# Kernel tuning notes

Measured on AMD Instinct MI355X. Metric: run time of the kernel, lower is better.

Reference implementation:

```python
import jax, jax.numpy as jnp
import numpy as np

N_TOKENS = 524288
D = 128          # input_dim == output_dim (output = zeros_like(x))
E = 8            # num_experts


def setup_inputs() -> dict:
    key = jax.random.key(0)
    ks = jax.random.split(key, 5)
    s = 1.0 / np.sqrt(D)
    x = jax.random.normal(ks[0], (N_TOKENS, D), dtype=jnp.float32)
    gate_W = jax.random.uniform(ks[1], (E, D), jnp.float32, -s, s)   # Linear(D, E) weight [out,in]
    gate_b = jax.random.uniform(ks[2], (E,), jnp.float32, -s, s)
    W = jax.random.uniform(ks[3], (E, D, D), jnp.float32, -s, s)     # per-expert Linear weight [E, out, in]
    b = jax.random.uniform(ks[4], (E, D), jnp.float32, -s, s)
    return {"x": x, "gate_W": gate_W, "gate_b": gate_b, "W": W, "b": b}


def reference(x, gate_W, gate_b, W, b):
    # gate_scores: [N, E]
    g = jax.nn.softmax(x @ gate_W.T + gate_b, axis=-1)
    # top-2 expert mask per token: [N, E] float {0,1}
    _, top2 = jax.lax.top_k(g, 2)                                   # [N, 2] int
    mask = jnp.zeros_like(g).at[jnp.arange(x.shape[0])[:, None], top2].set(1.0)
    # Faithful to the loop: out = sum_e g[:,e] * ((mask_e * x) @ W_e^T + b_e)
    # contraction term:   einsum over expert e and feature d
    out = jnp.einsum('ne,nd,efd->nf', g * mask, x, W)
    out = out + g @ b                                               # bias term: every expert's bias, weighted by gate
    return out
```

## Files before the change

### kernel.cpp

```cpp
#include <hip/hip_runtime.h>


typedef _Float16 half8 __attribute__((ext_vector_type(8)));
typedef float    f32x4 __attribute__((ext_vector_type(4)));

#define N_TOK   524288
#define TPB     256

__global__ __launch_bounds__(512, 2)
void moe_fused(const float* __restrict__ x,
               const float* __restrict__ gW,
               const float* __restrict__ gb,
               const float* __restrict__ W,
               const float* __restrict__ b,
               float* __restrict__ out)
{
    const int tid  = threadIdx.x;
    const int lane = tid & 63;
    const int wid  = tid >> 6;
    const int wm   = wid >> 1;
    const int wn   = wid & 1;
    const int r16  = lane & 15;
    const int q    = lane >> 4;

    const int  t0w = wm * 64;
    const long tb  = (long)blockIdx.x * TPB;

    __shared__ __align__(16) float     gW_s[8 * 128];
    __shared__             float       gb_s[8];
    __shared__ __align__(16) float     c_s[8][256];
    __shared__ __align__(16) _Float16  gA_s[256 * 32];
    __shared__ __align__(16) _Float16  bB_s[128 * 32];
    __shared__ __align__(16) _Float16  wb_s[2][128 * 128];

    ((float2*)gW_s)[tid] = ((const float2*)gW)[tid];
    if (tid < 8) gb_s[tid] = gb[tid];
    for (int i = tid; i < 128 * 32; i += 512) {
        int f = i >> 5, k = i & 31;
        bB_s[i] = (k < 8) ? (_Float16)b[k * 128 + f] : (_Float16)0.f;
    }
    __syncthreads();

    f32x4 st[4][2];
    {
        const f32x4* wsrc = (const f32x4*)W;
        #pragma unroll
        for (int it = 0; it < 4; ++it) {
            int v = it * 512 + tid;
            st[it][0] = wsrc[v * 2 + 0];
            st[it][1] = wsrc[v * 2 + 1];
        }
    }

    half8 af[4][4];
    float plog[4][8];
    #pragma unroll
    for (int m = 0; m < 4; ++m)
        #pragma unroll
        for (int e = 0; e < 8; ++e) plog[m][e] = 0.f;

    #pragma unroll
    for (int m = 0; m < 4; ++m) {
        const long tok = tb + t0w + m * 16 + r16;
        const float* xr = x + tok * 128;
        #pragma unroll
        for (int k = 0; k < 4; ++k) {
            const int col = k * 32 + q * 8;
            f32x4 v0 = *(const f32x4*)(xr + col);
            f32x4 v1 = *(const f32x4*)(xr + col + 4);
            half8 pk;
            pk[0]=(_Float16)v0[0]; pk[1]=(_Float16)v0[1]; pk[2]=(_Float16)v0[2]; pk[3]=(_Float16)v0[3];
            pk[4]=(_Float16)v1[0]; pk[5]=(_Float16)v1[1]; pk[6]=(_Float16)v1[2]; pk[7]=(_Float16)v1[3];
            af[m][k] = pk;
            #pragma unroll
            for (int e = 0; e < 8; ++e) {
                const float* g = gW_s + e * 128 + col;
                plog[m][e] += v0[0]*g[0] + v0[1]*g[1] + v0[2]*g[2] + v0[3]*g[3]
                            + v1[0]*g[4] + v1[1]*g[5] + v1[2]*g[6] + v1[3]*g[7];
            }
        }
    }

    #pragma unroll
    for (int m = 0; m < 4; ++m) {
        #pragma unroll
        for (int e = 0; e < 8; ++e) {
            float v = plog[m][e];
            v += __shfl_xor(v, 16, 64);
            v += __shfl_xor(v, 32, 64);
            plog[m][e] = v + gb_s[e];
        }
        float m1 = -1e30f; int i1 = 0;
        #pragma unroll
        for (int e = 0; e < 8; ++e) if (plog[m][e] > m1) { m1 = plog[m][e]; i1 = e; }
        float m2 = -1e30f; int i2 = (i1 == 0) ? 1 : 0;
        #pragma unroll
        for (int e = 0; e < 8; ++e) if (e != i1 && plog[m][e] > m2) { m2 = plog[m][e]; i2 = e; }
        float ge[8]; float sum = 0.f;
        #pragma unroll
        for (int e = 0; e < 8; ++e) { ge[e] = __expf(plog[m][e] - m1); sum += ge[e]; }
        const float inv = 1.f / sum;
        if (q == 0 && wn == 0) {
            const int row = t0w + m * 16 + r16;
            half8 pg;
            #pragma unroll
            for (int e = 0; e < 8; ++e) {
                float gg = ge[e] * inv;
                c_s[e][row] = (e == i1 || e == i2) ? gg : 0.f;
                pg[e] = (_Float16)gg;
            }
            half8* gp = (half8*)&gA_s[row * 32];
            half8 z8 = {0,0,0,0,0,0,0,0};
            gp[0] = pg; gp[1] = z8; gp[2] = z8; gp[3] = z8;
        }
    }
    __syncthreads();

    f32x4 acc[4][4];
    const f32x4 zq = {0.f, 0.f, 0.f, 0.f};
    {
        half8 ga[4];
        #pragma unroll
        for (int m = 0; m < 4; ++m)
            ga[m] = *(const half8*)&gA_s[(t0w + m * 16 + r16) * 32 + q * 8];
        #pragma unroll
        for (int n = 0; n < 4; ++n) {
            const half8 bf = *(const half8*)&bB_s[(wn * 64 + n * 16 + r16) * 32 + q * 8];
            #pragma unroll
            for (int m = 0; m < 4; ++m)
                acc[m][n] = __builtin_amdgcn_mfma_f32_16x16x32_f16(ga[m], bf, zq, 0, 0, 0);
        }
    }

    #pragma unroll
    for (int it = 0; it < 4; ++it) {
        int v = it * 512 + tid;
        int f = v >> 4, slot = v & 15;
        char* dst = (char*)wb_s[0] + f * 256 + ((slot * 16) ^ ((f & 7) << 4));
        half8 pk;
        pk[0]=(_Float16)st[it][0][0]; pk[1]=(_Float16)st[it][0][1];
        pk[2]=(_Float16)st[it][0][2]; pk[3]=(_Float16)st[it][0][3];
        pk[4]=(_Float16)st[it][1][0]; pk[5]=(_Float16)st[it][1][1];
        pk[6]=(_Float16)st[it][1][2]; pk[7]=(_Float16)st[it][1][3];
        *(half8*)dst = pk;
    }
    __syncthreads();

    for (int e = 0; e < 8; ++e) {
        _Float16* wcur = wb_s[e & 1];
        _Float16* wnxt = wb_s[(e & 1) ^ 1];

        if (e < 7) {
            const f32x4* wsrc = (const f32x4*)(W + (long)(e + 1) * 16384);
            #pragma unroll
            for (int it = 0; it < 4; ++it) {
                int v = it * 512 + tid;
                st[it][0] = wsrc[v * 2 + 0];
                st[it][1] = wsrc[v * 2 + 1];
            }
        }

        f32x4 cv[4];
        #pragma unroll
        for (int m = 0; m < 4; ++m)
            cv[m] = *(const f32x4*)&c_s[e][t0w + m * 16 + q * 4];

        #pragma unroll
        for (int n = 0; n < 4; ++n) {
            const int fbase = wn * 64 + n * 16 + r16;
            const char* wrow = (const char*)wcur + fbase * 256;
            const int sw = (fbase & 7) << 4;
            f32x4 tmp[4];
            #pragma unroll
            for (int k = 0; k < 4; ++k) {
                const half8 bf = *(const half8*)(wrow + ((k * 64 + q * 16) ^ sw));
                #pragma unroll
                for (int m = 0; m < 4; ++m)
                    tmp[m] = __builtin_amdgcn_mfma_f32_16x16x32_f16(
                                 af[m][k], bf, (k == 0) ? zq : tmp[m], 0, 0, 0);
            }
            #pragma unroll
            for (int m = 0; m < 4; ++m) {
                acc[m][n][0] += cv[m][0] * tmp[m][0];
                acc[m][n][1] += cv[m][1] * tmp[m][1];
                acc[m][n][2] += cv[m][2] * tmp[m][2];
                acc[m][n][3] += cv[m][3] * tmp[m][3];
            }
        }

        if (e < 7) {
            #pragma unroll
            for (int it = 0; it < 4; ++it) {
                int v = it * 512 + tid;
                int f = v >> 4, slot = v & 15;
                char* dst = (char*)wnxt + f * 256 + ((slot * 16) ^ ((f & 7) << 4));
                half8 pk;
                pk[0]=(_Float16)st[it][0][0]; pk[1]=(_Float16)st[it][0][1];
                pk[2]=(_Float16)st[it][0][2]; pk[3]=(_Float16)st[it][0][3];
                pk[4]=(_Float16)st[it][1][0]; pk[5]=(_Float16)st[it][1][1];
                pk[6]=(_Float16)st[it][1][2]; pk[7]=(_Float16)st[it][1][3];
                *(half8*)dst = pk;
            }
            __syncthreads();
        }
    }

    #pragma unroll
    for (int m = 0; m < 4; ++m) {
        const long trow = tb + t0w + m * 16 + q * 4;
        #pragma unroll
        for (int r = 0; r < 4; ++r) {
            float* orow = out + (trow + r) * 128 + wn * 64 + r16;
            orow[0]  = acc[m][0][r];
            orow[16] = acc[m][1][r];
            orow[32] = acc[m][2][r];
            orow[48] = acc[m][3][r];
        }
    }
}

extern "C" void kernel_launch(void* const* d_in, const int* in_sizes, int n_in,
                              void* d_out, int out_size, void* d_ws, size_t ws_size,
                              hipStream_t stream) {
    const float* x  = (const float*)d_in[0];
    const float* gW = (const float*)d_in[1];
    const float* gb = (const float*)d_in[2];
    const float* W  = (const float*)d_in[3];
    const float* b  = (const float*)d_in[4];
    float* out = (float*)d_out;
    (void)in_sizes; (void)n_in; (void)out_size; (void)d_ws; (void)ws_size;

    moe_fused<<<dim3(N_TOK / TPB), dim3(512), 0, stream>>>(x, gW, gb, W, b, out);
}
```

Baseline: 2.106 ms.

## Pre-convert expert weights to fp16 and stage them via async global-to-LDS loads

A small pre-kernel converts W to fp16 in the workspace on every call. The main kernel then stages each expert's weights straight into LDS with global_load_lds, using a swizzled source address. This removes the register round-trip, the per-block fp32→fp16 conversion and the halved-width traffic of reading fp32 weights in every block. It adds a second launch and depends on the async load being complete before the existing barrier, with no explicit vmcnt wait, and register staging is dropped which may change occupancy.

```diff
diff --git a/kernel.cpp b/kernel.cpp
--- a/kernel.cpp
+++ b/kernel.cpp
@@ -2,16 +2,33 @@
 
 
 typedef _Float16 half8 __attribute__((ext_vector_type(8)));
+typedef _Float16 half4 __attribute__((ext_vector_type(4)));
 typedef float    f32x4 __attribute__((ext_vector_type(4)));
 
 #define N_TOK   524288
 #define TPB     256
 
-__global__ __launch_bounds__(512, 2)
+__device__ __forceinline__ void async_load16(const void* g, void* l) {
+    __builtin_amdgcn_global_load_lds(
+        (const __attribute__((address_space(1))) unsigned int*)g,
+        (__attribute__((address_space(3))) unsigned int*)l, 16, 0, 0);
+}
+
+__global__ __launch_bounds__(256)
+void convert_w(const float* __restrict__ W, _Float16* __restrict__ Wh) {
+    const int i = blockIdx.x * 256 + threadIdx.x;
+    f32x4 v = ((const f32x4*)W)[i];
+    half4 h;
+    h[0] = (_Float16)v[0]; h[1] = (_Float16)v[1];
+    h[2] = (_Float16)v[2]; h[3] = (_Float16)v[3];
+    ((half4*)Wh)[i] = h;
+}
+
+__global__ __launch_bounds__(512) __attribute__((amdgpu_waves_per_eu(2, 2)))
 void moe_fused(const float* __restrict__ x,
                const float* __restrict__ gW,
                const float* __restrict__ gb,
-               const float* __restrict__ W,
+               const _Float16* __restrict__ Wh,
                const float* __restrict__ b,
                float* __restrict__ out)
 {
@@ -33,24 +50,26 @@
     __shared__ __align__(16) _Float16  bB_s[128 * 32];
     __shared__ __align__(16) _Float16  wb_s[2][128 * 128];
 
+    auto stage = [&](int e, int bufidx) {
+        const _Float16* base = Wh + e * 16384;
+        char* lbase = (char*)wb_s[bufidx];
+        #pragma unroll
+        for (int it = 0; it < 4; ++it) {
+            const int v = it * 512 + tid;
+            const int f = v >> 4, u = v & 15;
+            async_load16(base + f * 128 + ((u ^ (f & 7)) * 8), lbase + v * 16);
+        }
+    };
+
     ((float2*)gW_s)[tid] = ((const float2*)gW)[tid];
     if (tid < 8) gb_s[tid] = gb[tid];
     for (int i = tid; i < 128 * 32; i += 512) {
         int f = i >> 5, k = i & 31;
         bB_s[i] = (k < 8) ? (_Float16)b[k * 128 + f] : (_Float16)0.f;
     }
+
+    stage(0, 0);
     __syncthreads();
-
-    f32x4 st[4][2];
-    {
-        const f32x4* wsrc = (const f32x4*)W;
-        #pragma unroll
-        for (int it = 0; it < 4; ++it) {
-            int v = it * 512 + tid;
-            st[it][0] = wsrc[v * 2 + 0];
-            st[it][1] = wsrc[v * 2 + 1];
-        }
-    }
 
     half8 af[4][4];
     float plog[4][8];
@@ -132,33 +151,10 @@
         }
     }
 
-    #pragma unroll
-    for (int it = 0; it < 4; ++it) {
-        int v = it * 512 + tid;
-        int f = v >> 4, slot = v & 15;
-        char* dst = (char*)wb_s[0] + f * 256 + ((slot * 16) ^ ((f & 7) << 4));
-        half8 pk;
-        pk[0]=(_Float16)st[it][0][0]; pk[1]=(_Float16)st[it][0][1];
-        pk[2]=(_Float16)st[it][0][2]; pk[3]=(_Float16)st[it][0][3];
-        pk[4]=(_Float16)st[it][1][0]; pk[5]=(_Float16)st[it][1][1];
-        pk[6]=(_Float16)st[it][1][2]; pk[7]=(_Float16)st[it][1][3];
-        *(half8*)dst = pk;
-    }
-    __syncthreads();
-
     for (int e = 0; e < 8; ++e) {
-        _Float16* wcur = wb_s[e & 1];
-        _Float16* wnxt = wb_s[(e & 1) ^ 1];
-
-        if (e < 7) {
-            const f32x4* wsrc = (const f32x4*)(W + (long)(e + 1) * 16384);
-            #pragma unroll
-            for (int it = 0; it < 4; ++it) {
-                int v = it * 512 + tid;
-                st[it][0] = wsrc[v * 2 + 0];
-                st[it][1] = wsrc[v * 2 + 1];
-            }
-        }
+        const _Float16* wcur = wb_s[e & 1];
+
+        if (e < 7) stage(e + 1, (e & 1) ^ 1);
 
         f32x4 cv[4];
         #pragma unroll
@@ -188,21 +184,7 @@
             }
         }
 
-        if (e < 7) {
-            #pragma unroll
-            for (int it = 0; it < 4; ++it) {
-                int v = it * 512 + tid;
-                int f = v >> 4, slot = v & 15;
-                char* dst = (char*)wnxt + f * 256 + ((slot * 16) ^ ((f & 7) << 4));
-                half8 pk;
-                pk[0]=(_Float16)st[it][0][0]; pk[1]=(_Float16)st[it][0][1];
-                pk[2]=(_Float16)st[it][0][2]; pk[3]=(_Float16)st[it][0][3];
-                pk[4]=(_Float16)st[it][1][0]; pk[5]=(_Float16)st[it][1][1];
-                pk[6]=(_Float16)st[it][1][2]; pk[7]=(_Float16)st[it][1][3];
-                *(half8*)dst = pk;
-            }
-            __syncthreads();
-        }
+        if (e < 7) __syncthreads();
     }
 
     #pragma unroll
@@ -228,7 +210,9 @@
     const float* W  = (const float*)d_in[3];
     const float* b  = (const float*)d_in[4];
     float* out = (float*)d_out;
-    (void)in_sizes; (void)n_in; (void)out_size; (void)d_ws; (void)ws_size;
-
-    moe_fused<<<dim3(N_TOK / TPB), dim3(512), 0, stream>>>(x, gW, gb, W, b, out);
-}
+    _Float16* Wh = (_Float16*)d_ws;
+    (void)in_sizes; (void)n_in; (void)out_size; (void)ws_size;
+
+    convert_w<<<dim3(128), dim3(256), 0, stream>>>(W, Wh);
+    moe_fused<<<dim3(N_TOK / TPB), dim3(512), 0, stream>>>(x, gW, gb, Wh, b, out);
+}
```

Result: faster. 1.982 ms (-5.9%).
